# Kernel optimization log

Hardware: AMD Instinct MI355X
Metric: run time of the kernel (lower is better)

## Reference

```python
import math
import jax, jax.numpy as jnp
import numpy as np

B, S, HID = 1, 2048, 2048
H, D = 32, 64            # heads, head_dim = HID // H
THETA = 10000.0
EPS = 1e-6
LAYER_IDX = 12
LAM_INIT = 0.8 - 0.6 * math.exp(-0.3 * LAYER_IDX)  # lambda_init_fn(layer_idx)
SCALE = 1.0 / math.sqrt(D)


def _rope_cos_sin(seq_len, dim):
    inv_freq = 1.0 / (THETA ** (np.arange(0, dim, 2, dtype=np.float64) / dim))
    freqs = np.outer(np.arange(seq_len, dtype=np.float64), inv_freq)
    emb = np.concatenate([freqs, freqs], axis=-1)  # [S, D] (llama duplicates freqs)
    return jnp.asarray(np.cos(emb), jnp.float32), jnp.asarray(np.sin(emb), jnp.float32)


def _rotate_half(x):
    return jnp.concatenate([-x[..., D // 2:], x[..., : D // 2]], axis=-1)


def _apply_rope(x, cos, sin):
    # x: [B, H, S, D]; cos/sin: [S, D] broadcast over B, H
    return x * cos + _rotate_half(x) * sin


def setup_inputs() -> dict:
    key = jax.random.key(0)
    ks = jax.random.split(key, 10)
    return {
        "hidden_states": jax.random.normal(ks[0], (B, S, HID), jnp.float32),
        "Wq": jax.random.normal(ks[1], (2 * HID, HID), jnp.float32) * 0.02,
        "Wk": jax.random.normal(ks[2], (2 * HID, HID), jnp.float32) * 0.02,
        "Wv": jax.random.normal(ks[3], (HID, HID), jnp.float32) * 0.02,
        "Wo": jax.random.normal(ks[4], (HID, HID), jnp.float32) * 0.02,
        "lambda_q1": jax.random.normal(ks[5], (D,), jnp.float32) * 0.1,
        "lambda_k1": jax.random.normal(ks[6], (D,), jnp.float32) * 0.1,
        "lambda_q2": jax.random.normal(ks[7], (D,), jnp.float32) * 0.1,
        "lambda_k2": jax.random.normal(ks[8], (D,), jnp.float32) * 0.1,
        "subln_w": jnp.ones((D,), jnp.float32),
    }


def reference(hidden_states, Wq, Wk, Wv, Wo,
              lambda_q1, lambda_k1, lambda_q2, lambda_k2, subln_w):
    # Projections (nn.Linear, no bias): x @ W.T
    q = hidden_states @ Wq.T                       # [B, S, 2*HID]
    k = hidden_states @ Wk.T                       # [B, S, 2*HID]
    v = hidden_states @ Wv.T                       # [B, S, HID]

    def to_heads(t):  # [B, S, H*D] -> [B, H, S, D]
        return t.reshape(B, S, H, D).transpose(0, 2, 1, 3)

    q1, q2 = jnp.split(q, 2, axis=-1)
    k1, k2 = jnp.split(k, 2, axis=-1)
    q1, q2, k1, k2, v = map(to_heads, (q1, q2, k1, k2, v))

    cos, sin = _rope_cos_sin(S, D)
    q1, k1 = _apply_rope(q1, cos, sin), _apply_rope(k1, cos, sin)
    q2, k2 = _apply_rope(q2, cos, sin), _apply_rope(k2, cos, sin)

    # Causal additive mask [S, S]
    causal = jnp.tril(jnp.ones((S, S), bool))
    neg_inf = jnp.finfo(jnp.float32).min
    mask = jnp.where(causal, 0.0, neg_inf)

    s1 = jnp.einsum("bhqd,bhkd->bhqk", q1, k1) * SCALE + mask
    s2 = jnp.einsum("bhqd,bhkd->bhqk", q2, k2) * SCALE + mask

    lam = (jnp.exp(jnp.sum(lambda_q1 * lambda_k1))
           - jnp.exp(jnp.sum(lambda_q2 * lambda_k2)) + LAM_INIT)

    attn_w = jax.nn.softmax(s1, axis=-1) - lam * jax.nn.softmax(s2, axis=-1)
    attn = jnp.einsum("bhqk,bhkd->bhqd", attn_w, v)  # [B, H, S, D]

    # Head-wise RMSNorm (LlamaRMSNorm over value_head_dim)
    var = jnp.mean(jnp.square(attn), axis=-1, keepdims=True)
    attn = attn * jax.lax.rsqrt(var + EPS) * subln_w
    attn = attn * (1.0 - LAM_INIT)

    out = attn.transpose(0, 2, 1, 3).reshape(B, S, HID) @ Wo.T
    return out
```

## Files before the change

### kernel.cpp

```cpp
#include <hip/hip_runtime.h>


typedef __bf16 bf16;
typedef __bf16 bf16x4 __attribute__((ext_vector_type(4)));
typedef __bf16 bf16x8 __attribute__((ext_vector_type(8)));
typedef float  f32x4  __attribute__((ext_vector_type(4)));

#define MFMA(a, b, c) __builtin_amdgcn_mfma_f32_16x16x32_bf16((a), (b), (c), 0, 0, 0)

#define S_LEN   2048
#define HID_DIM 2048
#define NHEAD   32
#define HD      64
#define QKV_N   10240
#define LAM_INIT 0.7836057665316245f
#define ONE_MINUS_LAM_INIT 0.21639423346837553f
#define QSCALE  0.18033688011112042f
#define RMS_EPS 1e-6f
#define L2T     0.4152410118609203f

__device__ __forceinline__ void gld16(const void* g, void* l) {
    __builtin_amdgcn_global_load_lds(
        (const __attribute__((address_space(1))) void*)g,
        (__attribute__((address_space(3))) void*)l, 16, 0, 0);
}

__global__ void cvt_all(const float* __restrict__ hs, const float* __restrict__ Wq,
                        const float* __restrict__ Wk, const float* __restrict__ Wv,
                        const float* __restrict__ Wo,
                        const float* __restrict__ lq1, const float* __restrict__ lk1,
                        const float* __restrict__ lq2, const float* __restrict__ lk2,
                        bf16* __restrict__ hsb, bf16* __restrict__ Wb,
                        bf16* __restrict__ Wob, float* __restrict__ lam_out) {
    const int bid = blockIdx.x;
    if (bid >= 28672) {
        const int t = threadIdx.x;
        if (t < 64) {
            float a = lq1[t] * lk1[t];
            float b = lq2[t] * lk2[t];
            #pragma unroll
            for (int off = 32; off > 0; off >>= 1) {
                a += __shfl_xor(a, off, 64);
                b += __shfl_xor(b, off, 64);
            }
            if (t == 0) lam_out[0] = expf(a) - expf(b) + LAM_INIT;
        }
        return;
    }
    const float* src; bf16* dst; int off;
    if      (bid <  4096) { src = hs; dst = hsb;            off = bid;         }
    else if (bid < 12288) { src = Wq; dst = Wb;             off = bid - 4096;  }
    else if (bid < 20480) { src = Wk; dst = Wb +  8388608;  off = bid - 12288; }
    else if (bid < 24576) { src = Wv; dst = Wb + 16777216;  off = bid - 20480; }
    else                  { src = Wo; dst = Wob;            off = bid - 24576; }
    const int i = off * 1024 + threadIdx.x * 4;
    float4 v = *(const float4*)(src + i);
    bf16x4 o = { (bf16)v.x, (bf16)v.y, (bf16)v.z, (bf16)v.w };
    *(bf16x4*)(dst + i) = o;
}

__global__ __launch_bounds__(256, 3)
void qkv_rope_gemm(const bf16* __restrict__ A, const bf16* __restrict__ B,
                   bf16* __restrict__ Q1, bf16* __restrict__ Q2,
                   bf16* __restrict__ K1, bf16* __restrict__ K2,
                   bf16* __restrict__ Vt) {
    __shared__ __align__(16) bf16 As[128 * 64];
    __shared__ __align__(16) bf16 Bs[128 * 64];
    const int tid  = threadIdx.x;
    const int wave = tid >> 6, lane = tid & 63;
    const int wm = wave >> 1, wn = wave & 1;
    const int l = lane & 15, quad = lane >> 4;
    const int m0 = blockIdx.y * 128, n0 = blockIdx.x * 128;

    f32x4 acc[4][4];
    #pragma unroll
    for (int i = 0; i < 4; ++i)
        #pragma unroll
        for (int j = 0; j < 4; ++j) acc[i][j] = (f32x4){0.f, 0.f, 0.f, 0.f};

    const int rr  = tid >> 3;
    const int csw = ((tid & 7) ^ (rr & 7)) * 8;
    const bf16* Ag = A + (size_t)(m0 + rr) * HID_DIM + csw;
    const bf16* Bg = B + (size_t)(n0 + rr) * HID_DIM + csw;

    for (int kt = 0; kt < HID_DIM; kt += 64) {
        __syncthreads();
        #pragma unroll
        for (int j = 0; j < 4; ++j) {
            gld16(Ag + (size_t)(32 * j) * HID_DIM + kt, As + j * 2048 + tid * 8);
            gld16(Bg + (size_t)(32 * j) * HID_DIM + kt, Bs + j * 2048 + tid * 8);
        }
        __syncthreads();

        #pragma unroll
        for (int ks = 0; ks < 2; ++ks) {
            const int co = (((ks << 2) | quad) ^ (l & 7)) << 3;
            bf16x8 hf[4], wf[4];
            #pragma unroll
            for (int hi = 0; hi < 4; ++hi)
                hf[hi] = *(const bf16x8*)(As + (wm * 64 + hi * 16 + l) * 64 + co);
            #pragma unroll
            for (int wi = 0; wi < 4; ++wi)
                wf[wi] = *(const bf16x8*)(Bs + (wn * 64 + wi * 16 + l) * 64 + co);
            #pragma unroll
            for (int wi = 0; wi < 4; ++wi)
                #pragma unroll
                for (int hi = 0; hi < 4; ++hi)
                    acc[wi][hi] = MFMA(wf[wi], hf[hi], acc[wi][hi]);
        }
    }

    const int c = n0 + wn * 64;
    const int sbase = m0 + wm * 64;
    bf16* dst; int off; float scale = 1.0f; bool isv = false;
    if      (c < 2048) { dst = Q1; off = c;        scale = QSCALE; }
    else if (c < 4096) { dst = Q2; off = c - 2048; scale = QSCALE; }
    else if (c < 6144) { dst = K1; off = c - 4096; }
    else if (c < 8192) { dst = K2; off = c - 6144; }
    else               { isv = true; off = c - 8192; }
    const int h = off >> 6;

    if (!isv) {
        float invf[2][4];
        #pragma unroll
        for (int p = 0; p < 2; ++p)
            #pragma unroll
            for (int r = 0; r < 4; ++r)
                invf[p][r] = exp2f(-(float)(p * 16 + quad * 4 + r) * L2T);

        #pragma unroll
        for (int hi = 0; hi < 4; ++hi) {
            const float s = (float)(sbase + hi * 16 + l);
            float cs[2][4], sn[2][4];
            #pragma unroll
            for (int p = 0; p < 2; ++p)
                #pragma unroll
                for (int r = 0; r < 4; ++r) {
                    const float ang = s * invf[p][r];
                    cs[p][r] = __cosf(ang);
                    sn[p][r] = __sinf(ang);
                }
            bf16* rowp = dst + ((size_t)h * S_LEN + sbase + hi * 16 + l) * HD + quad * 4;
            #pragma unroll
            for (int wi = 0; wi < 4; ++wi) {
                const int p = wi & 1;
                const float sign = (wi < 2) ? -1.0f : 1.0f;
                bf16x4 o;
                #pragma unroll
                for (int r = 0; r < 4; ++r)
                    o[r] = (bf16)((acc[wi][hi][r] * cs[p][r] +
                                   sign * acc[wi ^ 2][hi][r] * sn[p][r]) * scale);
                *(bf16x4*)(rowp + wi * 16) = o;
            }
        }
    } else {
        #pragma unroll
        for (int wi = 0; wi < 4; ++wi)
            #pragma unroll
            for (int r = 0; r < 4; ++r) {
                bf16* vrow = Vt + ((size_t)h * HD + wi * 16 + quad * 4 + r) * S_LEN + sbase;
                #pragma unroll
                for (int hi = 0; hi < 4; ++hi)
                    vrow[hi * 16 + l] = (bf16)acc[wi][hi][r];
            }
    }
}

__global__ __launch_bounds__(256, 3)
void gemm_bt_splitk(const bf16* __restrict__ A, const bf16* __restrict__ B,
                    float* __restrict__ Cout, int M, int N, int K_total, int K_part) {
    __shared__ __align__(16) bf16 As[128 * 64];
    __shared__ __align__(16) bf16 Bs[128 * 64];
    const int tid  = threadIdx.x;
    const int wave = tid >> 6, lane = tid & 63;
    const int wm = wave >> 1, wn = wave & 1;
    const int l = lane & 15, quad = lane >> 4;
    const int m0 = blockIdx.y * 128, n0 = blockIdx.x * 128;
    const int kz = blockIdx.z * K_part;

    f32x4 acc[4][4];
    #pragma unroll
    for (int i = 0; i < 4; ++i)
        #pragma unroll
        for (int j = 0; j < 4; ++j) acc[i][j] = (f32x4){0.f, 0.f, 0.f, 0.f};

    const int rr  = tid >> 3;
    const int csw = ((tid & 7) ^ (rr & 7)) * 8;
    const bf16* Ag = A + (size_t)(m0 + rr) * K_total + kz + csw;
    const bf16* Bg = B + (size_t)(n0 + rr) * K_total + kz + csw;

    for (int kt = 0; kt < K_part; kt += 64) {
        __syncthreads();
        #pragma unroll
        for (int j = 0; j < 4; ++j) {
            gld16(Ag + (size_t)(32 * j) * K_total + kt, As + j * 2048 + tid * 8);
            gld16(Bg + (size_t)(32 * j) * K_total + kt, Bs + j * 2048 + tid * 8);
        }
        __syncthreads();

        #pragma unroll
        for (int ks = 0; ks < 2; ++ks) {
            const int co = (((ks << 2) | quad) ^ (l & 7)) << 3;
            bf16x8 af[4], bfr[4];
            #pragma unroll
            for (int mi = 0; mi < 4; ++mi)
                af[mi] = *(const bf16x8*)(As + (wm * 64 + mi * 16 + l) * 64 + co);
            #pragma unroll
            for (int ni = 0; ni < 4; ++ni)
                bfr[ni] = *(const bf16x8*)(Bs + (wn * 64 + ni * 16 + l) * 64 + co);
            #pragma unroll
            for (int mi = 0; mi < 4; ++mi)
                #pragma unroll
                for (int ni = 0; ni < 4; ++ni)
                    acc[mi][ni] = MFMA(af[mi], bfr[ni], acc[mi][ni]);
        }
    }

    float* Pf = Cout + (size_t)blockIdx.z * M * N;
    #pragma unroll
    for (int mi = 0; mi < 4; ++mi)
        #pragma unroll
        for (int ni = 0; ni < 4; ++ni)
            #pragma unroll
            for (int r = 0; r < 4; ++r) {
                const int row = m0 + wm * 64 + mi * 16 + quad * 4 + r;
                const int col = n0 + wn * 64 + ni * 16 + l;
                Pf[(size_t)row * N + col] = acc[mi][ni][r];
            }
}

__global__ void reduce_add(const float* __restrict__ p, float* __restrict__ out, int n) {
    const int i = (blockIdx.x * 256 + threadIdx.x) * 4;
    float4 a = *(const float4*)(p + i);
    float4 b = *(const float4*)(p + n + i);
    float4 o = { a.x + b.x, a.y + b.y, a.z + b.z, a.w + b.w };
    *(float4*)(out + i) = o;
}

__global__ __launch_bounds__(256, 2)
void diff_attn(const bf16* __restrict__ Q1, const bf16* __restrict__ K1,
               const bf16* __restrict__ Q2, const bf16* __restrict__ K2,
               const bf16* __restrict__ Vt, const float* __restrict__ lam_p,
               const float* __restrict__ subln_w, bf16* __restrict__ attn_out) {
    const int bid  = blockIdx.x;
    const int h    = (bid >> 1) & 31;
    const int idx  = bid >> 6;
    const int qb   = (bid & 1) ? idx : (15 - idx);
    const int q0   = qb * 128;
    const int tid  = threadIdx.x;
    const int wave = tid >> 6, lane = tid & 63;
    const int sid  = wave >> 1, half = wave & 1;
    const int l    = lane & 15, quad = lane >> 4;
    const int q0w  = q0 + half * 64;

    __shared__ __align__(16) char smem[61440];
    bf16* K1s = (bf16*)smem;
    bf16* K2s = (bf16*)(smem + 8192);
    bf16* Vts = (bf16*)(smem + 16384);
    bf16* Pw  = (bf16*)(smem + 24576 + wave * 9216);

    const bf16* Qh  = (sid ? Q2 : Q1) + ((size_t)h * S_LEN + q0w) * HD;
    const bf16* K1g = K1 + (size_t)h * S_LEN * HD;
    const bf16* K2g = K2 + (size_t)h * S_LEN * HD;
    const bf16* Vtg = Vt + (size_t)h * HD * S_LEN;
    const bf16* Ksm = sid ? K2s : K1s;

    const int rr  = tid >> 3;
    const int csw = ((tid & 7) ^ (rr & 7)) * 8;
    bf16* l1 = K1s + tid * 8;
    bf16* l2 = K2s + tid * 8;
    bf16* lv = Vts + tid * 8;

    bf16x8 qf[4][2];
    #pragma unroll
    for (int ni = 0; ni < 4; ++ni)
        #pragma unroll
        for (int ks = 0; ks < 2; ++ks)
            qf[ni][ks] = *(const bf16x8*)(Qh + (ni * 16 + l) * HD + ks * 32 + quad * 8);

    f32x4 O[4][4];
    #pragma unroll
    for (int mi = 0; mi < 4; ++mi)
        #pragma unroll
        for (int ni = 0; ni < 4; ++ni)
            O[mi][ni] = (f32x4){0.f, 0.f, 0.f, 0.f};
    float csum[4] = {0.f, 0.f, 0.f, 0.f};

    const int T = 2 * qb + 2;
    const int sw8 = l & 7;
    for (int t = 0; t < T; ++t) {
        const int kv0 = t * 64;
        __syncthreads();
        {
            const bf16* k1p = K1g + (size_t)(kv0 + rr) * HD + csw;
            const bf16* k2p = K2g + (size_t)(kv0 + rr) * HD + csw;
            const bf16* vtp = Vtg + (size_t)rr * S_LEN + kv0 + csw;
            gld16(k1p, l1);
            gld16(k1p + (size_t)32 * HD, l1 + 2048);
            gld16(k2p, l2);
            gld16(k2p + (size_t)32 * HD, l2 + 2048);
            gld16(vtp, lv);
            gld16(vtp + (size_t)32 * S_LEN, lv + 2048);
        }
        __syncthreads();

        if (kv0 <= q0w) {
            const bool diag = (kv0 == q0w);

            #pragma unroll
            for (int mi = 0; mi < 4; ++mi) {
                const int krow = (mi * 16 + l) * 64;
                bf16x8 ka0 = *(const bf16x8*)(Ksm + krow + ((quad ^ sw8) << 3));
                bf16x8 ka1 = *(const bf16x8*)(Ksm + krow + (((4 + quad) ^ sw8) << 3));
                #pragma unroll
                for (int ni = 0; ni < 4; ++ni) {
                    f32x4 c = (f32x4){0.f, 0.f, 0.f, 0.f};
                    c = MFMA(ka0, qf[ni][0], c);
                    c = MFMA(ka1, qf[ni][1], c);
                    bf16x4 pk;
                    float lsum = 0.f;
                    #pragma unroll
                    for (int r = 0; r < 4; ++r) {
                        float p = __builtin_amdgcn_exp2f(c[r]);
                        if (diag && (mi * 16 + quad * 4 + r > ni * 16 + l)) p = 0.f;
                        lsum += p;
                        pk[r] = (bf16)p;
                    }
                    csum[ni] += lsum;
                    *(bf16x4*)(Pw + (ni * 16 + l) * 72 + mi * 16 + quad * 4) = pk;
                }
            }

            bf16x8 vb[2][4];
            #pragma unroll
            for (int ks = 0; ks < 2; ++ks)
                #pragma unroll
                for (int ni = 0; ni < 4; ++ni)
                    vb[ks][ni] = *(const bf16x8*)(Vts + (ni * 16 + l) * 64 +
                                                  ((((ks << 2) + quad) ^ sw8) << 3));

            asm volatile("s_waitcnt lgkmcnt(0)" ::: "memory");

            #pragma unroll
            for (int ks = 0; ks < 2; ++ks) {
                bf16x8 pa[4];
                #pragma unroll
                for (int mi = 0; mi < 4; ++mi)
                    pa[mi] = *(const bf16x8*)(Pw + (mi * 16 + l) * 72 + ks * 32 + quad * 8);
                #pragma unroll
                for (int ni = 0; ni < 4; ++ni)
                    #pragma unroll
                    for (int mi = 0; mi < 4; ++mi)
                        O[mi][ni] = MFMA(pa[mi], vb[ks][ni], O[mi][ni]);
            }
        }
    }

    __syncthreads();
    float* epi = (float*)(smem + half * 16640);

    #pragma unroll
    for (int ni = 0; ni < 4; ++ni) {
        csum[ni] += __shfl_xor(csum[ni], 16, 64);
        csum[ni] += __shfl_xor(csum[ni], 32, 64);
    }

    if (sid == 1) {
        const float lam = lam_p[0];
        #pragma unroll
        for (int mi = 0; mi < 4; ++mi)
            #pragma unroll
            for (int r = 0; r < 4; ++r) {
                const float inv = lam / __shfl(csum[mi], quad * 4 + r, 64);
                const int row = mi * 16 + quad * 4 + r;
                #pragma unroll
                for (int ni = 0; ni < 4; ++ni)
                    epi[row * 65 + ni * 16 + l] = O[mi][ni][r] * inv;
            }
    }
    __syncthreads();

    if (sid == 0) {
        float sw[4];
        #pragma unroll
        for (int ni = 0; ni < 4; ++ni) sw[ni] = subln_w[ni * 16 + l];

        #pragma unroll
        for (int mi = 0; mi < 4; ++mi) {
            float inv1[4];
            #pragma unroll
            for (int r = 0; r < 4; ++r)
                inv1[r] = 1.0f / __shfl(csum[mi], quad * 4 + r, 64);

            float v[4][4]; float ssq[4] = {0.f, 0.f, 0.f, 0.f};
            #pragma unroll
            for (int ni = 0; ni < 4; ++ni)
                #pragma unroll
                for (int r = 0; r < 4; ++r) {
                    const int row = mi * 16 + quad * 4 + r;
                    const float x = O[mi][ni][r] * inv1[r] - epi[row * 65 + ni * 16 + l];
                    v[ni][r] = x;
                    ssq[r] += x * x;
                }
            #pragma unroll
            for (int r = 0; r < 4; ++r) {
                float s = ssq[r];
                s += __shfl_xor(s, 1, 64);
                s += __shfl_xor(s, 2, 64);
                s += __shfl_xor(s, 4, 64);
                s += __shfl_xor(s, 8, 64);
                ssq[r] = rsqrtf(s * (1.0f / 64.0f) + RMS_EPS) * ONE_MINUS_LAM_INIT;
            }
            #pragma unroll
            for (int ni = 0; ni < 4; ++ni)
                #pragma unroll
                for (int r = 0; r < 4; ++r) {
                    const int row = q0w + mi * 16 + quad * 4 + r;
                    attn_out[(size_t)row * HID_DIM + h * 64 + ni * 16 + l] =
                        (bf16)(v[ni][r] * ssq[r] * sw[ni]);
                }
        }
    }
}

extern "C" void kernel_launch(void* const* d_in, const int* in_sizes, int n_in,
                              void* d_out, int out_size, void* d_ws, size_t ws_size,
                              hipStream_t stream) {
    const float* hs  = (const float*)d_in[0];
    const float* Wq  = (const float*)d_in[1];
    const float* Wk  = (const float*)d_in[2];
    const float* Wv  = (const float*)d_in[3];
    const float* Wo  = (const float*)d_in[4];
    const float* lq1 = (const float*)d_in[5];
    const float* lk1 = (const float*)d_in[6];
    const float* lq2 = (const float*)d_in[7];
    const float* lk2 = (const float*)d_in[8];
    const float* slw = (const float*)d_in[9];

    if (ws_size < 151000000u) return;

    char* ws = (char*)d_ws;
    bf16*  hsb  = (bf16*)(ws);
    bf16*  Wb   = (bf16*)(ws + 8388608);
    bf16*  Wob  = (bf16*)(ws + 50331648);
    float* part = (float*)(ws + 58720256);
    bf16*  Q1b  = (bf16*)(ws + 100663296);
    bf16*  K1b  = (bf16*)(ws + 109051904);
    bf16*  Q2b  = (bf16*)(ws + 117440512);
    bf16*  K2b  = (bf16*)(ws + 125829120);
    bf16*  Vtb  = (bf16*)(ws + 134217728);
    bf16*  abuf = (bf16*)(ws + 142606336);
    float* lamp = (float*)(ws + 150994944);

    cvt_all<<<28673, 256, 0, stream>>>(hs, Wq, Wk, Wv, Wo, lq1, lk1, lq2, lk2,
                                       hsb, Wb, Wob, lamp);

    qkv_rope_gemm<<<dim3(QKV_N / 128, S_LEN / 128), 256, 0, stream>>>(
        hsb, Wb, Q1b, Q2b, K1b, K2b, Vtb);

    diff_attn<<<512, 256, 0, stream>>>(Q1b, K1b, Q2b, K2b, Vtb, lamp, slw, abuf);

    gemm_bt_splitk<<<dim3(HID_DIM / 128, S_LEN / 128, 2), 256, 0, stream>>>(
        abuf, Wob, part, S_LEN, HID_DIM, HID_DIM, HID_DIM / 2);
    reduce_add<<<4096, 256, 0, stream>>>(part, (float*)d_out, S_LEN * HID_DIM);
}
```

Before: 363.0 us.

## Double-buffer K/V tiles and keep P in registers via permlane swaps

Splits the shared K1/K2/Vt staging into two buffers so the next tile's global-to-LDS loads run while the current tile computes, leaving one barrier per iteration. The P matrix no longer round-trips through per-wave LDS scratch; it is packed with v_cvt_pk_bf16_f32 and rearranged into MFMA operand layout with permlane32/16 swaps, with a shuffle fallback. It also adds s_setprio around the MFMA block. Cost: more registers held live for K and V fragments and the dependence on the permlane builtins; the epilogue's smem reuse must still fit the smaller allocation.

Result: no change. 359.0 us (-1.1%).

```diff
diff --git a/kernel.cpp b/kernel.cpp
--- a/kernel.cpp
+++ b/kernel.cpp
@@ -5,6 +5,9 @@
 typedef __bf16 bf16x4 __attribute__((ext_vector_type(4)));
 typedef __bf16 bf16x8 __attribute__((ext_vector_type(8)));
 typedef float  f32x4  __attribute__((ext_vector_type(4)));
+typedef unsigned int u32;
+typedef u32 u32x2 __attribute__((ext_vector_type(2)));
+typedef u32 u32x4 __attribute__((ext_vector_type(4)));
 
 #define MFMA(a, b, c) __builtin_amdgcn_mfma_f32_16x16x32_bf16((a), (b), (c), 0, 0, 0)
 
@@ -23,6 +26,24 @@
     __builtin_amdgcn_global_load_lds(
         (const __attribute__((address_space(1))) void*)g,
         (__attribute__((address_space(3))) void*)l, 16, 0, 0);
+}
+
+__device__ __forceinline__ void pa_build(u32 x, u32 y, int quad, u32& wlo, u32& whi) {
+#if __has_builtin(__builtin_amdgcn_permlane32_swap) && __has_builtin(__builtin_amdgcn_permlane16_swap)
+    u32x2 s = __builtin_amdgcn_permlane32_swap(x, y, false, false);
+    u32x2 t = __builtin_amdgcn_permlane16_swap(s.x, s.y, false, false);
+    wlo = t.x;
+    whi = t.y;
+#else
+    const u32 x16 = (u32)__shfl_xor((int)x, 16, 64);
+    const u32 x32 = (u32)__shfl_xor((int)x, 32, 64);
+    const u32 x48 = (u32)__shfl_xor((int)x, 48, 64);
+    const u32 y16 = (u32)__shfl_xor((int)y, 16, 64);
+    const u32 y32 = (u32)__shfl_xor((int)y, 32, 64);
+    const u32 y48 = (u32)__shfl_xor((int)y, 48, 64);
+    wlo = (quad == 0) ? x   : (quad == 1) ? x48 : (quad == 2) ? y32 : y16;
+    whi = (quad == 0) ? x16 : (quad == 1) ? x32 : (quad == 2) ? y48 : y;
+#endif
 }
 
 __global__ void cvt_all(const float* __restrict__ hs, const float* __restrict__ Wq,
@@ -253,116 +274,136 @@
     const int l    = lane & 15, quad = lane >> 4;
     const int q0w  = q0 + half * 64;
 
-    __shared__ __align__(16) char smem[61440];
-    bf16* K1s = (bf16*)smem;
-    bf16* K2s = (bf16*)(smem + 8192);
-    bf16* Vts = (bf16*)(smem + 16384);
-    bf16* Pw  = (bf16*)(smem + 24576 + wave * 9216);
+    __shared__ __align__(16) char smem[49152];
 
     const bf16* Qh  = (sid ? Q2 : Q1) + ((size_t)h * S_LEN + q0w) * HD;
     const bf16* K1g = K1 + (size_t)h * S_LEN * HD;
     const bf16* K2g = K2 + (size_t)h * S_LEN * HD;
     const bf16* Vtg = Vt + (size_t)h * HD * S_LEN;
-    const bf16* Ksm = sid ? K2s : K1s;
 
     const int rr  = tid >> 3;
     const int csw = ((tid & 7) ^ (rr & 7)) * 8;
-    bf16* l1 = K1s + tid * 8;
-    bf16* l2 = K2s + tid * 8;
-    bf16* lv = Vts + tid * 8;
+    const int sw8 = l & 7;
+
+    auto stage = [&](int kv, int bufb) {
+        const bf16* k1p = K1g + (size_t)(kv + rr) * HD + csw;
+        const bf16* k2p = K2g + (size_t)(kv + rr) * HD + csw;
+        const bf16* vtp = Vtg + (size_t)rr * S_LEN + kv + csw;
+        bf16* d1 = (bf16*)(smem + bufb)         + tid * 8;
+        bf16* d2 = (bf16*)(smem + bufb + 8192)  + tid * 8;
+        bf16* dv = (bf16*)(smem + bufb + 16384) + tid * 8;
+        gld16(k1p,                       d1);
+        gld16(k1p + (size_t)32 * HD,     d1 + 2048);
+        gld16(k2p,                       d2);
+        gld16(k2p + (size_t)32 * HD,     d2 + 2048);
+        gld16(vtp,                       dv);
+        gld16(vtp + (size_t)32 * S_LEN,  dv + 2048);
+    };
 
     bf16x8 qf[4][2];
     #pragma unroll
-    for (int ni = 0; ni < 4; ++ni)
+    for (int g = 0; g < 4; ++g)
         #pragma unroll
         for (int ks = 0; ks < 2; ++ks)
-            qf[ni][ks] = *(const bf16x8*)(Qh + (ni * 16 + l) * HD + ks * 32 + quad * 8);
+            qf[g][ks] = *(const bf16x8*)(Qh + (g * 16 + l) * HD + ks * 32 + quad * 8);
 
     f32x4 O[4][4];
     #pragma unroll
-    for (int mi = 0; mi < 4; ++mi)
-        #pragma unroll
-        for (int ni = 0; ni < 4; ++ni)
-            O[mi][ni] = (f32x4){0.f, 0.f, 0.f, 0.f};
+    for (int g = 0; g < 4; ++g)
+        #pragma unroll
+        for (int nd = 0; nd < 4; ++nd)
+            O[g][nd] = (f32x4){0.f, 0.f, 0.f, 0.f};
     float csum[4] = {0.f, 0.f, 0.f, 0.f};
 
     const int T = 2 * qb + 2;
-    const int sw8 = l & 7;
+
+    stage(0, 0);
+    asm volatile("s_waitcnt vmcnt(0)" ::: "memory");
+    __builtin_amdgcn_s_barrier();
+
     for (int t = 0; t < T; ++t) {
         const int kv0 = t * 64;
-        __syncthreads();
-        {
-            const bf16* k1p = K1g + (size_t)(kv0 + rr) * HD + csw;
-            const bf16* k2p = K2g + (size_t)(kv0 + rr) * HD + csw;
-            const bf16* vtp = Vtg + (size_t)rr * S_LEN + kv0 + csw;
-            gld16(k1p, l1);
-            gld16(k1p + (size_t)32 * HD, l1 + 2048);
-            gld16(k2p, l2);
-            gld16(k2p + (size_t)32 * HD, l2 + 2048);
-            gld16(vtp, lv);
-            gld16(vtp + (size_t)32 * S_LEN, lv + 2048);
-        }
-        __syncthreads();
+        const int bb  = (t & 1) * 24576;
+
+        if (t + 1 < T) stage(kv0 + 64, 24576 - bb);
 
         if (kv0 <= q0w) {
             const bool diag = (kv0 == q0w);
-
-            #pragma unroll
-            for (int mi = 0; mi < 4; ++mi) {
-                const int krow = (mi * 16 + l) * 64;
-                bf16x8 ka0 = *(const bf16x8*)(Ksm + krow + ((quad ^ sw8) << 3));
-                bf16x8 ka1 = *(const bf16x8*)(Ksm + krow + (((4 + quad) ^ sw8) << 3));
-                #pragma unroll
-                for (int ni = 0; ni < 4; ++ni) {
-                    f32x4 c = (f32x4){0.f, 0.f, 0.f, 0.f};
-                    c = MFMA(ka0, qf[ni][0], c);
-                    c = MFMA(ka1, qf[ni][1], c);
-                    bf16x4 pk;
-                    float lsum = 0.f;
+            const bf16* Ksm = (const bf16*)(smem + bb + (sid ? 8192 : 0));
+            const bf16* Vts = (const bf16*)(smem + bb + 16384);
+
+            bf16x8 ka[4][2];
+            #pragma unroll
+            for (int mk = 0; mk < 4; ++mk) {
+                const int krow = (mk * 16 + l) * 64;
+                ka[mk][0] = *(const bf16x8*)(Ksm + krow + ((quad ^ sw8) << 3));
+                ka[mk][1] = *(const bf16x8*)(Ksm + krow + (((4 + quad) ^ sw8) << 3));
+            }
+            bf16x8 vb[2][4];
+            #pragma unroll
+            for (int ks = 0; ks < 2; ++ks)
+                #pragma unroll
+                for (int nd = 0; nd < 4; ++nd)
+                    vb[ks][nd] = *(const bf16x8*)(Vts + (nd * 16 + l) * 64 +
+                                                  ((((ks << 2) + quad) ^ sw8) << 3));
+
+            __builtin_amdgcn_s_setprio(1);
+            #pragma unroll
+            for (int g = 0; g < 4; ++g) {
+                f32x4 c[4];
+                #pragma unroll
+                for (int mk = 0; mk < 4; ++mk) {
+                    c[mk] = (f32x4){0.f, 0.f, 0.f, 0.f};
+                    c[mk] = MFMA(ka[mk][0], qf[g][0], c[mk]);
+                    c[mk] = MFMA(ka[mk][1], qf[g][1], c[mk]);
+                }
+                u32 dw[4][2];
+                float lsum = 0.f;
+                #pragma unroll
+                for (int mk = 0; mk < 4; ++mk) {
+                    float p[4];
                     #pragma unroll
                     for (int r = 0; r < 4; ++r) {
-                        float p = __builtin_amdgcn_exp2f(c[r]);
-                        if (diag && (mi * 16 + quad * 4 + r > ni * 16 + l)) p = 0.f;
-                        lsum += p;
-                        pk[r] = (bf16)p;
+                        p[r] = __builtin_amdgcn_exp2f(c[mk][r]);
+                        if (diag && (mk * 16 + quad * 4 + r > g * 16 + l)) p[r] = 0.f;
+                        lsum += p[r];
                     }
-                    csum[ni] += lsum;
-                    *(bf16x4*)(Pw + (ni * 16 + l) * 72 + mi * 16 + quad * 4) = pk;
+                    asm("v_cvt_pk_bf16_f32 %0, %1, %2" : "=v"(dw[mk][0]) : "v"(p[0]), "v"(p[1]));
+                    asm("v_cvt_pk_bf16_f32 %0, %1, %2" : "=v"(dw[mk][1]) : "v"(p[2]), "v"(p[3]));
                 }
-            }
-
-            bf16x8 vb[2][4];
-            #pragma unroll
-            for (int ks = 0; ks < 2; ++ks)
-                #pragma unroll
-                for (int ni = 0; ni < 4; ++ni)
-                    vb[ks][ni] = *(const bf16x8*)(Vts + (ni * 16 + l) * 64 +
-                                                  ((((ks << 2) + quad) ^ sw8) << 3));
-
-            asm volatile("s_waitcnt lgkmcnt(0)" ::: "memory");
-
-            #pragma unroll
-            for (int ks = 0; ks < 2; ++ks) {
-                bf16x8 pa[4];
-                #pragma unroll
-                for (int mi = 0; mi < 4; ++mi)
-                    pa[mi] = *(const bf16x8*)(Pw + (mi * 16 + l) * 72 + ks * 32 + quad * 8);
-                #pragma unroll
-                for (int ni = 0; ni < 4; ++ni)
-                    #pragma unroll
-                    for (int mi = 0; mi < 4; ++mi)
-                        O[mi][ni] = MFMA(pa[mi], vb[ks][ni], O[mi][ni]);
-            }
-        }
+                csum[g] += lsum;
+
+                u32 wa0, wa1, wa2, wa3, wb0, wb1, wb2, wb3;
+                pa_build(dw[0][0], dw[1][0], quad, wa0, wa2);
+                pa_build(dw[0][1], dw[1][1], quad, wa1, wa3);
+                pa_build(dw[2][0], dw[3][0], quad, wb0, wb2);
+                pa_build(dw[2][1], dw[3][1], quad, wb1, wb3);
+                u32x4 w0 = {wa0, wa1, wa2, wa3};
+                u32x4 w1 = {wb0, wb1, wb2, wb3};
+                bf16x8 pa0, pa1;
+                __builtin_memcpy(&pa0, &w0, 16);
+                __builtin_memcpy(&pa1, &w1, 16);
+
+                #pragma unroll
+                for (int nd = 0; nd < 4; ++nd) {
+                    O[g][nd] = MFMA(pa0, vb[0][nd], O[g][nd]);
+                    O[g][nd] = MFMA(pa1, vb[1][nd], O[g][nd]);
+                }
+            }
+            __builtin_amdgcn_s_setprio(0);
+        }
+
+        asm volatile("s_waitcnt vmcnt(0)" ::: "memory");
+        __builtin_amdgcn_s_barrier();
     }
 
     __syncthreads();
     float* epi = (float*)(smem + half * 16640);
 
     #pragma unroll
-    for (int ni = 0; ni < 4; ++ni) {
-        csum[ni] += __shfl_xor(csum[ni], 16, 64);
-        csum[ni] += __shfl_xor(csum[ni], 32, 64);
+    for (int g = 0; g < 4; ++g) {
+        csum[g] += __shfl_xor(csum[g], 16, 64);
+        csum[g] += __shfl_xor(csum[g], 32, 64);
     }
 
     if (sid == 1) {
```
